# Kernel tuning notes

Hardware: AMD Instinct MI355X
Metric: run time of the kernel (lower is better)

The kernel has to match this reference:

```python
import jax, jax.numpy as jnp
import numpy as np
from jax import lax

B, C, N, T, K = 16, 64, 512, 64, 3
EPS = 1e-5


def _bn(x, g, b):
    # training-mode BatchNorm2d over (B, H=N, W=T) per channel
    m = jnp.mean(x, axis=(0, 2, 3), keepdims=True)
    v = jnp.var(x, axis=(0, 2, 3), keepdims=True)
    return (x - m) * lax.rsqrt(v + EPS) * g[None, :, None, None] + b[None, :, None, None]


def _conv(x, w, b, pad):
    y = lax.conv_general_dilated(x, w, (1, 1), ((0, 0), pad),
                                 dimension_numbers=('NCHW', 'OIHW', 'NCHW'))
    return y + b[None, :, None, None]


def setup_inputs() -> dict:
    key = jax.random.key(0)
    ks = jax.random.split(key, 8)
    xav = lambda k, sh, fi, fo: jax.random.normal(k, sh, jnp.float32) * np.sqrt(2.0 / (fi + fo))
    return {
        'x': jax.random.normal(ks[0], (B, C, N, T), jnp.float32),
        'adj_mx': jax.random.normal(ks[1], (K, N, N), jnp.float32) / np.sqrt(N),
        'cheb_w': xav(ks[2], (K, C, C), C, C),
        'cheb_b': jnp.zeros((C,), jnp.float32),
        'w1': xav(ks[3], (C, C, 1, 3), 3 * C, 3 * C),
        'b1': jnp.zeros((C,), jnp.float32),
        'g1': jnp.ones((C,), jnp.float32),
        'be1': jnp.zeros((C,), jnp.float32),
        'w2': xav(ks[4], (C, C, 1, 3), 3 * C, 3 * C),
        'b2': jnp.zeros((C,), jnp.float32),
        'g2': jnp.ones((C,), jnp.float32),
        'be2': jnp.zeros((C,), jnp.float32),
        'gate_w': xav(ks[5], (C, 2 * C, 1, 1), 2 * C, C),
        'gate_b': jnp.zeros((C,), jnp.float32),
        'res_w': xav(ks[6], (C, C, 1, 1), C, C),
        'res_b': jnp.zeros((C,), jnp.float32),
        'g3': jnp.ones((C,), jnp.float32),
        'be3': jnp.zeros((C,), jnp.float32),
    }


def _forward(x, adj_mx, cheb_w, cheb_b, w1, b1, g1, be1, w2, b2, g2, be2,
             gate_w, gate_b, res_w, res_b, g3, be3):
    # ChebFilterBlock: out[b,o,n,t] = sum_{k,i,m} x[b,i,m,t] adj[k,m,n] W[k,i,o] + bias
    spatial = jnp.einsum('bimt,kmn,kio->bont', x, adj_mx, cheb_w) \
              + cheb_b[None, :, None, None]
    # temporal branch: two (1,3) convs with BN+ReLU
    t = jax.nn.relu(_bn(_conv(x, w1, b1, (1, 1)), g1, be1))
    t = jax.nn.relu(_bn(_conv(t, w2, b2, (1, 1)), g2, be2))
    # gated fusion
    comb = jnp.concatenate([spatial, t], axis=1)
    gate = jax.nn.sigmoid(_conv(comb, gate_w, gate_b, (0, 0)))
    res = _conv(x, res_w, res_b, (0, 0))
    out = gate * spatial + (1.0 - gate) * t + res
    return _bn(out, g3, be3)


def reference(x, adj_mx, cheb_w, cheb_b, w1, b1, g1, be1, w2, b2, g2, be2,
              gate_w, gate_b, res_w, res_b, g3, be3):
    return _forward(x, adj_mx, cheb_w, cheb_b, w1, b1, g1, be1, w2, b2, g2, be2,
                    gate_w, gate_b, res_w, res_b, g3, be3)
```

## Files before the change

### kernel.cpp

```cpp
#include <hip/hip_runtime.h>
#include <hip/hip_bf16.h>
#include <cstdint>

#define BB 16
#define CC 64
#define NN 512
#define TT 64
#define KCH 3
#define PP (BB*NN*TT)
#define EPSB 1e-5f

typedef __bf16 bf16;
typedef __bf16 bf16x8 __attribute__((ext_vector_type(8)));
typedef __bf16 bf16x4 __attribute__((ext_vector_type(4)));
typedef float  f32x4  __attribute__((ext_vector_type(4)));

#define MFMA16(A,Bv,Cv) __builtin_amdgcn_mfma_f32_16x16x32_bf16((A),(Bv),(Cv),0,0,0)

__device__ __forceinline__ void gload_lds16(const bf16* g, bf16* l){
  __builtin_amdgcn_global_load_lds(
      (const __attribute__((address_space(1))) void*)g,
      (__attribute__((address_space(3))) void*)l, 16, 0, 0);
}

__global__ __launch_bounds__(256) void k_adjT(const float* __restrict__ adj,
                                              bf16* __restrict__ adjb){
  int idx = blockIdx.x*256 + threadIdx.x;
  int m = idx & 511, n = (idx >> 9) & 511, k = idx >> 18;
  adjb[idx] = (bf16)adj[((size_t)(k*512 + m))*512 + n];
}

__global__ __launch_bounds__(256) void k_wprep(const float* __restrict__ w1,
    const float* __restrict__ w2, const float* __restrict__ cw,
    const float* __restrict__ gw, const float* __restrict__ rw,
    bf16* __restrict__ w1p, bf16* __restrict__ w2p, bf16* __restrict__ cp,
    bf16* __restrict__ gp, bf16* __restrict__ rp){
  int tid = threadIdx.x;
  for (int e = tid; e < 6*2048; e += 256){
    int j = e&7, lane = (e>>3)&63, cf = (e>>9)&3, ks = e>>11;
    int k = ks*32 + (lane>>4)*8 + j, col = cf*16 + (lane&15);
    int kk = k >> 6, i = k & 63;
    w1p[e] = (bf16)w1[(col*64 + i)*3 + kk];
    w2p[e] = (bf16)w2[(col*64 + i)*3 + kk];
    cp[e]  = (bf16)cw[((size_t)kk*64 + i)*64 + col];
  }
  for (int e = tid; e < 4*2048; e += 256){
    int j = e&7, lane = (e>>3)&63, cf = (e>>9)&3, ks = e>>11;
    int k = ks*32 + (lane>>4)*8 + j, col = cf*16 + (lane&15);
    gp[e] = (bf16)gw[col*128 + k];
  }
  for (int e = tid; e < 2*2048; e += 256){
    int j = e&7, lane = (e>>3)&63, cf = (e>>9)&3, ks = e>>11;
    int k = ks*32 + (lane>>4)*8 + j, col = cf*16 + (lane&15);
    rp[e] = (bf16)rw[col*64 + k];
  }
}

__global__ __launch_bounds__(256) void k_xlb(const float* __restrict__ x,
                                             bf16* __restrict__ xlb){
  __shared__ float tile[64][65];
  int bn = blockIdx.x; int b = bn >> 9, n = bn & 511;
  int tid = threadIdx.x;
  const float* xp = x + ((size_t)(b*64)*512 + n)*64;
  for (int p = 0; p < 4; ++p){
    int q = p*256 + tid;
    int i = q >> 4, tc = (q & 15)*4;
    float4 v = *reinterpret_cast<const float4*>(xp + (size_t)i*512*64 + tc);
    tile[i][tc+0] = v.x; tile[i][tc+1] = v.y; tile[i][tc+2] = v.z; tile[i][tc+3] = v.w;
  }
  __syncthreads();
  bf16* op = xlb + (size_t)bn*4096;
  for (int p = 0; p < 2; ++p){
    int v8 = p*256 + tid;
    int t = v8 >> 3, ic = (v8 & 7)*8;
    bf16x8 o;
    #pragma unroll
    for (int e = 0; e < 8; ++e) o[e] = (bf16)tile[ic+e][t];
    *reinterpret_cast<bf16x8*>(op + t*64 + ic) = o;
  }
}

__global__ __launch_bounds__(256) void k_xmt(const float* __restrict__ x,
                                             bf16* __restrict__ xmt){
  __shared__ bf16 lds[16][16][72];
  int bid = blockIdx.x;
  int t0 = (bid & 3)*16, m0 = ((bid>>2)&7)*64, i0 = ((bid>>5)&3)*16, b = bid>>7;
  int tid = threadIdx.x;
  int tq = tid & 3, m = tid >> 2;
  for (int i = 0; i < 16; ++i){
    float4 v = *reinterpret_cast<const float4*>(
        x + ((size_t)(b*64 + i0 + i)*512 + (m0 + m))*64 + t0 + tq*4);
    lds[tq*4+0][i][m] = (bf16)v.x; lds[tq*4+1][i][m] = (bf16)v.y;
    lds[tq*4+2][i][m] = (bf16)v.z; lds[tq*4+3][i][m] = (bf16)v.w;
  }
  __syncthreads();
  for (int p = 0; p < 8; ++p){
    int row = p*32 + (tid >> 3); int t = row >> 4, i = row & 15, mc = tid & 7;
    bf16x8 v = *reinterpret_cast<const bf16x8*>(&lds[t][i][mc*8]);
    *reinterpret_cast<bf16x8*>(
        xmt + ((size_t)((b*64 + t0 + t)*64) + i0 + i)*512 + m0 + mc*8) = v;
  }
}

__global__ __launch_bounds__(256,4) void k_conv(const bf16* __restrict__ in,
    const bf16* __restrict__ wp, bf16* __restrict__ outp, float* __restrict__ part,
    const float* __restrict__ sc, const float* __restrict__ sh){
  int tid = threadIdx.x, w = tid >> 6, l = tid & 63, l15 = l & 15, lg = l >> 4;
  int blk = blockIdx.x;
  size_t rowbase = (size_t)blk * 64;
  const bf16* xr = in + rowbase * 64;
  int t = w*16 + l15;
  f32x4 acc[4] = {};
  #pragma unroll
  for (int ks = 0; ks < 6; ++ks){
    int dt = ks >> 1, kh = ks & 1;
    int ts = t + dt - 1;
    bf16x8 a = {};
    if (ts >= 0 && ts < 64){
      a = *reinterpret_cast<const bf16x8*>(xr + ts*64 + kh*32 + lg*8);
      if (sc){
        int i0 = kh*32 + lg*8;
        #pragma unroll
        for (int e = 0; e < 8; ++e){
          float f = (float)a[e]*sc[i0+e] + sh[i0+e];
          a[e] = (bf16)fmaxf(f, 0.f);
        }
      }
    }
    #pragma unroll
    for (int cf = 0; cf < 4; ++cf){
      bf16x8 bfr = *reinterpret_cast<const bf16x8*>(wp + ((ks*4 + cf)*64 + l)*8);
      acc[cf] = MFMA16(a, bfr, acc[cf]);
    }
  }
  __shared__ float ssum[4][4][16], ssq[4][4][16];
  #pragma unroll
  for (int cf = 0; cf < 4; ++cf){
    int o = cf*16 + l15;
    float s = 0.f, q = 0.f;
    #pragma unroll
    for (int r = 0; r < 4; ++r){
      float vv = acc[cf][r];
      int to = w*16 + lg*4 + r;
      outp[(rowbase + to)*64 + o] = (bf16)vv;
      s += vv; q += vv*vv;
    }
    s += __shfl_xor(s, 16); s += __shfl_xor(s, 32);
    q += __shfl_xor(q, 16); q += __shfl_xor(q, 32);
    if (lg == 0){ ssum[w][cf][l15] = s; ssq[w][cf][l15] = q; }
  }
  __syncthreads();
  if (tid < 64){
    int cf = tid >> 4, c = tid & 15;
    float s = ssum[0][cf][c]+ssum[1][cf][c]+ssum[2][cf][c]+ssum[3][cf][c];
    float q = ssq[0][cf][c]+ssq[1][cf][c]+ssq[2][cf][c]+ssq[3][cf][c];
    part[(size_t)blk*128 + tid*2]     = s;
    part[(size_t)blk*128 + tid*2 + 1] = q;
  }
}

__global__ __launch_bounds__(256) void k_stats(const float* __restrict__ part, int nb,
    const float* __restrict__ g, const float* __restrict__ be,
    float* __restrict__ sc, float* __restrict__ sh){
  int c = blockIdx.x, tid = threadIdx.x;
  float s = 0.f, q = 0.f;
  for (int i = tid; i < nb; i += 256){
    s += part[(size_t)i*128 + c*2];
    q += part[(size_t)i*128 + c*2 + 1];
  }
  __shared__ float rs[256], rq[256];
  rs[tid] = s; rq[tid] = q; __syncthreads();
  for (int st = 128; st > 0; st >>= 1){
    if (tid < st){ rs[tid] += rs[tid+st]; rq[tid] += rq[tid+st]; }
    __syncthreads();
  }
  if (tid == 0){
    float cnt = (float)PP;
    float mean = rs[0]/cnt, var = rq[0]/cnt - mean*mean;
    float r = rsqrtf(var + EPSB);
    sc[c] = g[c]*r;
    sh[c] = be[c] - mean*g[c]*r;
  }
}

__global__ __launch_bounds__(256,2) void k_gemm1(const bf16* __restrict__ xmt,
    const bf16* __restrict__ adjb, const bf16* __restrict__ cp,
    const float* __restrict__ cb, bf16* __restrict__ spm){
  __shared__ bf16 As[3][128*32];
  __shared__ bf16 Bs[3][128*32];
  __shared__ bf16 VT[128*128];

  int tid = threadIdx.x, w = tid >> 6, l = tid & 63, l15 = l & 15, lg = l >> 4;
  int wr = w >> 1, wc = w & 1;

  int orig = blockIdx.x;
  int wg = (orig & 7) * 256 + (orig >> 3);
  int jt = wg >> 2, nt = wg & 3;
  int J0 = jt*128, N0 = nt*128;

  const bf16* aglob = xmt + (size_t)J0*512;

  auto stage = [&](int buf, int m0, const bf16* bg){
    #pragma unroll
    for (int p = 0; p < 2; ++p){
      int idx = p*256 + tid;
      int r = idx >> 2, c = idx & 3;
      int cg = c ^ (r & 3);
      gload_lds16(aglob + (size_t)r*512 + m0 + cg*8,
                  &As[buf][(p*256 + w*64)*8]);
      gload_lds16(bg + (size_t)r*512 + m0 + cg*8,
                  &Bs[buf][(p*256 + w*64)*8]);
    }
  };

  f32x4 acc2[4][4] = {};
  const bf16* bglob = adjb + (size_t)N0*512;
  stage(0, 0, bglob);
  stage(1, 32, bglob);

  int tw = w >> 1;
  for (int kk = 0; kk < 3; ++kk){
    f32x4 acc[4][4] = {};
    for (int ks = 0; ks < 16; ++ks){
      if (ks <= 13) stage((ks+2)%3, (ks+2)*32, bglob);
      if (ks <= 13)      asm volatile("s_waitcnt vmcnt(8)" ::: "memory");
      else if (ks == 14) asm volatile("s_waitcnt vmcnt(4)" ::: "memory");
      else               asm volatile("s_waitcnt vmcnt(0)" ::: "memory");
      __builtin_amdgcn_s_barrier();
      __builtin_amdgcn_sched_barrier(0);

      int cbuf = ks % 3;
      bf16x8 a[4], bb[4];
      #pragma unroll
      for (int rf = 0; rf < 4; ++rf){
        int row = wr*64 + rf*16 + l15;
        a[rf] = *reinterpret_cast<const bf16x8*>(
            &As[cbuf][row*32 + ((lg ^ (row & 3))*8)]);
      }
      #pragma unroll
      for (int cf = 0; cf < 4; ++cf){
        int row = wc*64 + cf*16 + l15;
        bb[cf] = *reinterpret_cast<const bf16x8*>(
            &Bs[cbuf][row*32 + ((lg ^ (row & 3))*8)]);
      }
      #pragma unroll
      for (int rf = 0; rf < 4; ++rf)
        #pragma unroll
        for (int cf = 0; cf < 4; ++cf)
          acc[rf][cf] = MFMA16(a[rf], bb[cf], acc[rf][cf]);

      asm volatile("s_waitcnt lgkmcnt(0)" ::: "memory");
      __builtin_amdgcn_sched_barrier(0);
      __builtin_amdgcn_s_barrier();
    }

    #pragma unroll
    for (int rf = 0; rf < 4; ++rf){
      int jb = wr*8 + rf*2 + (lg >> 1);
      #pragma unroll
      for (int cf = 0; cf < 4; ++cf){
        int n = wc*64 + cf*16 + l15;
        bf16x4 pk;
        #pragma unroll
        for (int r = 0; r < 4; ++r) pk[r] = (bf16)acc[rf][cf][r];
        *reinterpret_cast<bf16x4*>(
            &VT[n*128 + ((jb ^ (n & 15)) << 3) + ((lg & 1) << 2)]) = pk;
      }
    }
    if (kk < 2){
      bglob = adjb + ((size_t)(kk+1)*512 + N0)*512;
      stage(0, 0, bglob);
      stage(1, 32, bglob);
    }
    asm volatile("s_waitcnt lgkmcnt(0)" ::: "memory");
    __builtin_amdgcn_sched_barrier(0);
    __builtin_amdgcn_s_barrier();

    #pragma unroll
    for (int ks2 = 0; ks2 < 2; ++ks2){
      bf16x8 bc[4];
      #pragma unroll
      for (int cf = 0; cf < 4; ++cf)
        bc[cf] = *reinterpret_cast<const bf16x8*>(
            cp + (((kk*2 + ks2)*4 + cf)*64 + l)*8);
      #pragma unroll
      for (int rf = 0; rf < 4; ++rf){
        int n = (w & 1)*64 + rf*16 + l15;
        int jb = tw*8 + ks2*4 + lg;
        bf16x8 a2 = *reinterpret_cast<const bf16x8*>(
            &VT[n*128 + ((jb ^ (n & 15)) << 3)]);
        #pragma unroll
        for (int cf = 0; cf < 4; ++cf)
          acc2[rf][cf] = MFMA16(a2, bc[cf], acc2[rf][cf]);
      }
    }
    asm volatile("s_waitcnt lgkmcnt(0)" ::: "memory");
    __builtin_amdgcn_sched_barrier(0);
    __builtin_amdgcn_s_barrier();
  }

  bf16* SP = VT;
  float cbv[4];
  #pragma unroll
  for (int cf = 0; cf < 4; ++cf) cbv[cf] = cb[cf*16 + l15];
  #pragma unroll
  for (int rf = 0; rf < 4; ++rf){
    int rowb = w*64 + rf*16 + lg*4;
    #pragma unroll
    for (int cf = 0; cf < 4; ++cf){
      int o = cf*16 + l15;
      #pragma unroll
      for (int r = 0; r < 4; ++r)
        SP[(rowb + r)*64 + o] = (bf16)(acc2[rf][cf][r] + cbv[cf]);
    }
  }
  __syncthreads();
  int b = jt >> 5, t0 = (jt & 31)*2;
  #pragma unroll
  for (int q = 0; q < 8; ++q){
    int flat = q*256 + tid;
    int row = flat >> 3, oc = (flat & 7)*8;
    int tl = row >> 7, n = N0 + (row & 127);
    bf16x8 vv = *reinterpret_cast<const bf16x8*>(&SP[row*64 + oc]);
    *reinterpret_cast<bf16x8*>(
        &spm[(((size_t)b*512 + n)*64 + (t0 + tl))*64 + oc]) = vv;
  }
}

__global__ __launch_bounds__(256,4) void k_fusion(const bf16* __restrict__ spm,
    const bf16* __restrict__ t2, const bf16* __restrict__ xlb,
    const bf16* __restrict__ gp, const bf16* __restrict__ rp,
    const float* __restrict__ sc2, const float* __restrict__ sh2,
    const float* __restrict__ gateb, bf16* __restrict__ pre,
    float* __restrict__ part){
  int tid = threadIdx.x, w = tid >> 6, l = tid & 63, l15 = l & 15, lg = l >> 4;
  int blk = blockIdx.x;
  int b = blk >> 9, n = blk & 511;
  size_t rowbase = (size_t)blk * 64;
  int t = w*16 + l15;
  f32x4 ag[4] = {}, ar[4] = {};
  #pragma unroll
  for (int ks = 0; ks < 4; ++ks){
    bf16x8 a;
    if (ks < 2){
      a = *reinterpret_cast<const bf16x8*>(spm + (rowbase + t)*64 + ks*32 + lg*8);
    } else {
      int i0 = (ks-2)*32 + lg*8;
      bf16x8 raw = *reinterpret_cast<const bf16x8*>(t2 + (rowbase + t)*64 + i0);
      #pragma unroll
      for (int e = 0; e < 8; ++e){
        float f = (float)raw[e]*sc2[i0+e] + sh2[i0+e];
        a[e] = (bf16)fmaxf(f, 0.f);
      }
    }
    #pragma unroll
    for (int cf = 0; cf < 4; ++cf){
      bf16x8 bfr = *reinterpret_cast<const bf16x8*>(gp + ((ks*4 + cf)*64 + l)*8);
      ag[cf] = MFMA16(a, bfr, ag[cf]);
    }
  }
  #pragma unroll
  for (int ks = 0; ks < 2; ++ks){
    bf16x8 a = *reinterpret_cast<const bf16x8*>(xlb + (rowbase + t)*64 + ks*32 + lg*8);
    #pragma unroll
    for (int cf = 0; cf < 4; ++cf){
      bf16x8 bfr = *reinterpret_cast<const bf16x8*>(rp + ((ks*4 + cf)*64 + l)*8);
      ar[cf] = MFMA16(a, bfr, ar[cf]);
    }
  }
  __shared__ float ssum[4][4][16], ssq[4][4][16];
  int tb = w*16 + lg*4;
  #pragma unroll
  for (int cf = 0; cf < 4; ++cf){
    int o = cf*16 + l15;
    float gb = gateb[o], sco = sc2[o], sho = sh2[o];
    float s = 0.f, q = 0.f;
    bf16x4 ov;
    #pragma unroll
    for (int r = 0; r < 4; ++r){
      size_t row = rowbase + tb + r;
      float z = ag[cf][r] + gb;
      float g = 1.f/(1.f + __expf(-z));
      float spv = (float)spm[row*64 + o];
      float tv  = (float)t2[row*64 + o];
      tv = fmaxf(tv*sco + sho, 0.f);
      float val = g*spv + (1.f - g)*tv + ar[cf][r];
      ov[r] = (bf16)val;
      s += val; q += val*val;
    }
    *reinterpret_cast<bf16x4*>(pre + (((size_t)b*64 + o)*512 + n)*64 + tb) = ov;
    s += __shfl_xor(s, 16); s += __shfl_xor(s, 32);
    q += __shfl_xor(q, 16); q += __shfl_xor(q, 32);
    if (lg == 0){ ssum[w][cf][l15] = s; ssq[w][cf][l15] = q; }
  }
  __syncthreads();
  if (tid < 64){
    int cf = tid >> 4, c = tid & 15;
    float s = ssum[0][cf][c]+ssum[1][cf][c]+ssum[2][cf][c]+ssum[3][cf][c];
    float q = ssq[0][cf][c]+ssq[1][cf][c]+ssq[2][cf][c]+ssq[3][cf][c];
    part[(size_t)blk*128 + tid*2]     = s;
    part[(size_t)blk*128 + tid*2 + 1] = q;
  }
}

__global__ __launch_bounds__(256) void k_bn3(const bf16* __restrict__ pre,
    float* __restrict__ out,
    const float* __restrict__ sc, const float* __restrict__ sh){
  size_t total8 = (size_t)BB*CC*NN*TT/8;
  for (size_t i8 = (size_t)blockIdx.x*256 + threadIdx.x; i8 < total8;
       i8 += (size_t)gridDim.x*256){
    bf16x8 v = reinterpret_cast<const bf16x8*>(pre)[i8];
    int o = (int)(i8 >> 12) & 63;
    float a = sc[o], bsh = sh[o];
    float4 r0, r1;
    r0.x = (float)v[0]*a + bsh; r0.y = (float)v[1]*a + bsh;
    r0.z = (float)v[2]*a + bsh; r0.w = (float)v[3]*a + bsh;
    r1.x = (float)v[4]*a + bsh; r1.y = (float)v[5]*a + bsh;
    r1.z = (float)v[6]*a + bsh; r1.w = (float)v[7]*a + bsh;
    reinterpret_cast<float4*>(out)[i8*2]     = r0;
    reinterpret_cast<float4*>(out)[i8*2 + 1] = r1;
  }
}

extern "C" void kernel_launch(void* const* d_in, const int* in_sizes, int n_in,
                              void* d_out, int out_size, void* d_ws, size_t ws_size,
                              hipStream_t stream){
  (void)in_sizes; (void)n_in; (void)out_size; (void)ws_size;
  const float* x   = (const float*)d_in[0];
  const float* adj = (const float*)d_in[1];
  const float* cw  = (const float*)d_in[2];
  const float* cb  = (const float*)d_in[3];
  const float* w1  = (const float*)d_in[4];
  const float* g1  = (const float*)d_in[6];
  const float* be1 = (const float*)d_in[7];
  const float* w2  = (const float*)d_in[8];
  const float* g2  = (const float*)d_in[10];
  const float* be2 = (const float*)d_in[11];
  const float* gw  = (const float*)d_in[12];
  const float* gb  = (const float*)d_in[13];
  const float* rw  = (const float*)d_in[14];
  const float* g3  = (const float*)d_in[16];
  const float* be3 = (const float*)d_in[17];
  float* out = (float*)d_out;

  char* ws = (char*)d_ws;
  size_t off = 0;
  auto alloc = [&](size_t bytes)->char*{
    char* p = ws + off; off += (bytes + 255) & ~(size_t)255; return p;
  };
  bf16* xlb  = (bf16*)alloc((size_t)PP*64*2);
  bf16* xmt  = (bf16*)alloc((size_t)PP*64*2);
  bf16* t1   = (bf16*)alloc((size_t)PP*64*2);
  bf16* t2   = (bf16*)alloc((size_t)PP*64*2);
  bf16* spm  = t1;
  bf16* pre  = xmt;
  bf16* adjb = (bf16*)alloc((size_t)KCH*512*512*2);
  bf16* w1p  = (bf16*)alloc(6*2048*2);
  bf16* w2p  = (bf16*)alloc(6*2048*2);
  bf16* cp   = (bf16*)alloc(6*2048*2);
  bf16* gp   = (bf16*)alloc(4*2048*2);
  bf16* rp   = (bf16*)alloc(2*2048*2);
  float* part = (float*)alloc((size_t)8192*128*4);
  float* s1sc = (float*)alloc(256); float* s1sh = (float*)alloc(256);
  float* s2sc = (float*)alloc(256); float* s2sh = (float*)alloc(256);
  float* s3sc = (float*)alloc(256); float* s3sh = (float*)alloc(256);

  k_adjT <<<dim3(3072), dim3(256), 0, stream>>>(adj, adjb);
  k_wprep<<<dim3(1),    dim3(256), 0, stream>>>(w1, w2, cw, gw, rw, w1p, w2p, cp, gp, rp);
  k_xlb  <<<dim3(8192), dim3(256), 0, stream>>>(x, xlb);
  k_xmt  <<<dim3(2048), dim3(256), 0, stream>>>(x, xmt);

  k_conv <<<dim3(8192), dim3(256), 0, stream>>>(xlb, w1p, t1, part, nullptr, nullptr);
  k_stats<<<dim3(64),   dim3(256), 0, stream>>>(part, 8192, g1, be1, s1sc, s1sh);
  k_conv <<<dim3(8192), dim3(256), 0, stream>>>(t1, w2p, t2, part, s1sc, s1sh);
  k_stats<<<dim3(64),   dim3(256), 0, stream>>>(part, 8192, g2, be2, s2sc, s2sh);

  k_gemm1<<<dim3(2048), dim3(256), 0, stream>>>(xmt, adjb, cp, cb, spm);

  k_fusion<<<dim3(8192), dim3(256), 0, stream>>>(spm, t2, xlb, gp, rp,
                                                 s2sc, s2sh, gb, pre, part);
  k_stats<<<dim3(64),   dim3(256), 0, stream>>>(part, 8192, g3, be3, s3sc, s3sh);
  k_bn3  <<<dim3(2048), dim3(256), 0, stream>>>(pre, out, s3sc, s3sh);
}
```

Baseline: 623.0 us.

## Flatten Chebyshev GEMM into single 48-step pipeline with k-major LDS layout

Merges the three per-order K loops of the fused adjacency GEMM into one 48-iteration loop, so loads for the next Chebyshev order stream in without a pipeline drain and refill between orders. The prefetch depth drops from two tiles ahead to one ahead. The LDS tile layout changes from an XOR-swizzled row-major layout to a chunk-major layout where each 16-byte k-chunk is contiguous across rows. The shallower prefetch may expose more memory latency, and the new layout changes LDS bank-conflict behaviour on the fragment reads.

```diff
diff --git a/kernel.cpp b/kernel.cpp
--- a/kernel.cpp
+++ b/kernel.cpp
@@ -186,8 +186,8 @@
 __global__ __launch_bounds__(256,2) void k_gemm1(const bf16* __restrict__ xmt,
     const bf16* __restrict__ adjb, const bf16* __restrict__ cp,
     const float* __restrict__ cb, bf16* __restrict__ spm){
-  __shared__ bf16 As[3][128*32];
-  __shared__ bf16 Bs[3][128*32];
+  __shared__ bf16 As[3][4096];
+  __shared__ bf16 Bs[3][4096];
   __shared__ bf16 VT[128*128];
 
   int tid = threadIdx.x, w = tid >> 6, l = tid & 63, l15 = l & 15, lg = l >> 4;
@@ -199,104 +199,96 @@
   int J0 = jt*128, N0 = nt*128;
 
   const bf16* aglob = xmt + (size_t)J0*512;
-
-  auto stage = [&](int buf, int m0, const bf16* bg){
+  const bf16* bbase = adjb + (size_t)N0*512;
+
+  auto stage = [&](int t){
+    int buf = t % 3;
+    const bf16* bg = bbase + (size_t)(t >> 4)*512*512;
+    int m0 = (t & 15)*32;
     #pragma unroll
     for (int p = 0; p < 2; ++p){
-      int idx = p*256 + tid;
-      int r = idx >> 2, c = idx & 3;
-      int cg = c ^ (r & 3);
-      gload_lds16(aglob + (size_t)r*512 + m0 + cg*8,
-                  &As[buf][(p*256 + w*64)*8]);
-      gload_lds16(bg + (size_t)r*512 + m0 + cg*8,
-                  &Bs[buf][(p*256 + w*64)*8]);
+      int q = p*256 + tid;
+      int r = q & 127, c = q >> 7;
+      gload_lds16(aglob + (size_t)r*512 + m0 + c*8, &As[buf][q*8]);
+      gload_lds16(bg    + (size_t)r*512 + m0 + c*8, &Bs[buf][q*8]);
     }
   };
 
   f32x4 acc2[4][4] = {};
-  const bf16* bglob = adjb + (size_t)N0*512;
-  stage(0, 0, bglob);
-  stage(1, 32, bglob);
-
+  f32x4 acc[4][4] = {};
   int tw = w >> 1;
-  for (int kk = 0; kk < 3; ++kk){
-    f32x4 acc[4][4] = {};
-    for (int ks = 0; ks < 16; ++ks){
-      if (ks <= 13) stage((ks+2)%3, (ks+2)*32, bglob);
-      if (ks <= 13)      asm volatile("s_waitcnt vmcnt(8)" ::: "memory");
-      else if (ks == 14) asm volatile("s_waitcnt vmcnt(4)" ::: "memory");
-      else               asm volatile("s_waitcnt vmcnt(0)" ::: "memory");
-      __builtin_amdgcn_s_barrier();
-      __builtin_amdgcn_sched_barrier(0);
-
-      int cbuf = ks % 3;
-      bf16x8 a[4], bb[4];
+
+  stage(0);
+  for (int t = 0; t < 48; ++t){
+    if (t < 47){
+      stage(t+1);
+      asm volatile("s_waitcnt vmcnt(4)" ::: "memory");
+    } else {
+      asm volatile("s_waitcnt vmcnt(0)" ::: "memory");
+    }
+    __builtin_amdgcn_s_barrier();
+    __builtin_amdgcn_sched_barrier(0);
+
+    int buf = t % 3;
+    bf16x8 a[4], bb[4];
+    #pragma unroll
+    for (int rf = 0; rf < 4; ++rf){
+      int row = wr*64 + rf*16 + l15;
+      a[rf] = *reinterpret_cast<const bf16x8*>(&As[buf][(lg*128 + row)*8]);
+    }
+    #pragma unroll
+    for (int cf = 0; cf < 4; ++cf){
+      int row = wc*64 + cf*16 + l15;
+      bb[cf] = *reinterpret_cast<const bf16x8*>(&Bs[buf][(lg*128 + row)*8]);
+    }
+    #pragma unroll
+    for (int rf = 0; rf < 4; ++rf)
+      #pragma unroll
+      for (int cf = 0; cf < 4; ++cf)
+        acc[rf][cf] = MFMA16(a[rf], bb[cf], acc[rf][cf]);
+
+    if ((t & 15) == 15){
+      int kk = t >> 4;
       #pragma unroll
       for (int rf = 0; rf < 4; ++rf){
-        int row = wr*64 + rf*16 + l15;
-        a[rf] = *reinterpret_cast<const bf16x8*>(
-            &As[cbuf][row*32 + ((lg ^ (row & 3))*8)]);
+        int jb = wr*8 + rf*2 + (lg >> 1);
+        #pragma unroll
+        for (int cf = 0; cf < 4; ++cf){
+          int n = wc*64 + cf*16 + l15;
+          bf16x4 pk;
+          #pragma unroll
+          for (int r = 0; r < 4; ++r) pk[r] = (bf16)acc[rf][cf][r];
+          *reinterpret_cast<bf16x4*>(
+              &VT[n*128 + ((jb ^ (n & 15)) << 3) + ((lg & 1) << 2)]) = pk;
+          acc[rf][cf] = (f32x4){0.f, 0.f, 0.f, 0.f};
+        }
       }
-      #pragma unroll
-      for (int cf = 0; cf < 4; ++cf){
-        int row = wc*64 + cf*16 + l15;
-        bb[cf] = *reinterpret_cast<const bf16x8*>(
-            &Bs[cbuf][row*32 + ((lg ^ (row & 3))*8)]);
-      }
-      #pragma unroll
-      for (int rf = 0; rf < 4; ++rf)
-        #pragma unroll
-        for (int cf = 0; cf < 4; ++cf)
-          acc[rf][cf] = MFMA16(a[rf], bb[cf], acc[rf][cf]);
-
       asm volatile("s_waitcnt lgkmcnt(0)" ::: "memory");
       __builtin_amdgcn_sched_barrier(0);
       __builtin_amdgcn_s_barrier();
-    }
-
-    #pragma unroll
-    for (int rf = 0; rf < 4; ++rf){
-      int jb = wr*8 + rf*2 + (lg >> 1);
+
       #pragma unroll
-      for (int cf = 0; cf < 4; ++cf){
-        int n = wc*64 + cf*16 + l15;
-        bf16x4 pk;
-        #pragma unroll
-        for (int r = 0; r < 4; ++r) pk[r] = (bf16)acc[rf][cf][r];
-        *reinterpret_cast<bf16x4*>(
-            &VT[n*128 + ((jb ^ (n & 15)) << 3) + ((lg & 1) << 2)]) = pk;
-      }
-    }
-    if (kk < 2){
-      bglob = adjb + ((size_t)(kk+1)*512 + N0)*512;
-      stage(0, 0, bglob);
-      stage(1, 32, bglob);
-    }
-    asm volatile("s_waitcnt lgkmcnt(0)" ::: "memory");
-    __builtin_amdgcn_sched_barrier(0);
-    __builtin_amdgcn_s_barrier();
-
-    #pragma unroll
-    for (int ks2 = 0; ks2 < 2; ++ks2){
-      bf16x8 bc[4];
-      #pragma unroll
-      for (int cf = 0; cf < 4; ++cf)
-        bc[cf] = *reinterpret_cast<const bf16x8*>(
-            cp + (((kk*2 + ks2)*4 + cf)*64 + l)*8);
-      #pragma unroll
-      for (int rf = 0; rf < 4; ++rf){
-        int n = (w & 1)*64 + rf*16 + l15;
-        int jb = tw*8 + ks2*4 + lg;
-        bf16x8 a2 = *reinterpret_cast<const bf16x8*>(
-            &VT[n*128 + ((jb ^ (n & 15)) << 3)]);
+      for (int ks2 = 0; ks2 < 2; ++ks2){
+        bf16x8 bc[4];
         #pragma unroll
         for (int cf = 0; cf < 4; ++cf)
-          acc2[rf][cf] = MFMA16(a2, bc[cf], acc2[rf][cf]);
+          bc[cf] = *reinterpret_cast<const bf16x8*>(
+              cp + (((kk*2 + ks2)*4 + cf)*64 + l)*8);
+        #pragma unroll
+        for (int rf = 0; rf < 4; ++rf){
+          int n = (w & 1)*64 + rf*16 + l15;
+          int jb = tw*8 + ks2*4 + lg;
+          bf16x8 a2 = *reinterpret_cast<const bf16x8*>(
+              &VT[n*128 + ((jb ^ (n & 15)) << 3)]);
+          #pragma unroll
+          for (int cf = 0; cf < 4; ++cf)
+            acc2[rf][cf] = MFMA16(a2, bc[cf], acc2[rf][cf]);
+        }
       }
-    }
-    asm volatile("s_waitcnt lgkmcnt(0)" ::: "memory");
-    __builtin_amdgcn_sched_barrier(0);
-    __builtin_amdgcn_s_barrier();
+      asm volatile("s_waitcnt lgkmcnt(0)" ::: "memory");
+      __builtin_amdgcn_sched_barrier(0);
+      __builtin_amdgcn_s_barrier();
+    }
   }
 
   bf16* SP = VT;
```

Result: slower. 674.8 us (+8.3%).
